# Optimization experiments

Measured on AMD Instinct MI355X. Metric: run time of the kernel, lower is better.

## Reference

```python
import jax, jax.numpy as jnp
import numpy as np

D_LINK = 64   # link_state_dim
D_PATH = 64   # path_state_dim
T = 3
MAX_LEN = 8   # max hops per path (max(seqs)+1)
R_UNITS = 256


def _glorot(k, shape):
    lim = np.sqrt(6.0 / (shape[0] + shape[-1])).astype(np.float32)
    return jax.random.uniform(k, shape, minval=-lim, maxval=lim, dtype=jnp.float32)


def setup_inputs() -> dict:
    key = jax.random.key(0)
    ks = jax.random.split(key, 16)
    n_links, n_paths, L = 50000, 100000, MAX_LEN
    capacities = jax.random.uniform(ks[0], (n_links,), dtype=jnp.float32) + 0.5
    traffic = jax.random.uniform(ks[1], (n_paths,), dtype=jnp.float32)
    # every path traverses L links; entries sorted by path id (tf.segment_sum assumption)
    paths = jnp.repeat(jnp.arange(n_paths, dtype=jnp.int32), L)
    seqs = jnp.tile(jnp.arange(L, dtype=jnp.int32), n_paths)
    links = jax.random.randint(ks[2], (n_paths * L,), 0, n_links, dtype=jnp.int32)
    return dict(
        capacities=capacities, traffic=traffic, links=links, paths=paths, seqs=seqs,
        Wx_p=_glorot(ks[3], (D_LINK, 3 * D_PATH)), Wh_p=_glorot(ks[4], (D_PATH, 3 * D_PATH)),
        b_p=jnp.zeros((3 * D_PATH,), jnp.float32),
        Wx_e=_glorot(ks[5], (D_PATH, 3 * D_LINK)), Wh_e=_glorot(ks[6], (D_LINK, 3 * D_LINK)),
        b_e=jnp.zeros((3 * D_LINK,), jnp.float32),
        W_r1=_glorot(ks[7], (D_PATH, R_UNITS)), b_r1=jnp.zeros((R_UNITS,), jnp.float32),
        W_r2=_glorot(ks[8], (R_UNITS, R_UNITS)), b_r2=jnp.zeros((R_UNITS,), jnp.float32),
        W_f=_glorot(ks[9], (D_PATH + R_UNITS, 1)), b_f=jnp.zeros((1,), jnp.float32),
        n_links=n_links, n_paths=n_paths,
    )


def gru_cell(x, h, Wx, Wh, b):
    # Keras GRUCell (reset_after=False), gate order z, r, h
    gx = x @ Wx + b
    gh = h @ Wh
    u = h.shape[-1]
    z = jax.nn.sigmoid(gx[..., :u] + gh[..., :u])
    r = jax.nn.sigmoid(gx[..., u:2 * u] + gh[..., u:2 * u])
    hc = jnp.tanh(gx[..., 2 * u:] + r * gh[..., 2 * u:])
    return z * h + (1.0 - z) * hc


def routenet_fwd(capacities, traffic, links, paths, seqs,
                 Wx_p, Wh_p, b_p, Wx_e, Wh_e, b_e,
                 W_r1, b_r1, W_r2, b_r2, W_f, b_f, n_links, n_paths):
    link_state = jnp.concatenate(
        [capacities[:, None], jnp.zeros((n_links, D_LINK - 1), capacities.dtype)], axis=1)
    path_state = jnp.concatenate(
        [traffic[:, None], jnp.zeros((n_paths, D_PATH - 1), traffic.dtype)], axis=1)
    lens = jax.ops.segment_sum(jnp.ones_like(paths), paths, num_segments=n_paths)  # [P]

    for _ in range(T):
        h_ = link_state[links]                                        # [E, D_LINK]
        link_inputs = jnp.zeros((n_paths, MAX_LEN, D_LINK), h_.dtype).at[paths, seqs].set(h_)

        def step(h, inp):
            xt, t = inp
            hn = gru_cell(xt, h, Wx_p, Wh_p, b_p)
            valid = (t < lens)[:, None]
            hn = jnp.where(valid, hn, h)          # dynamic_rnn copies state past seq len
            out = jnp.where(valid, hn, 0.0)       # and emits zeros there
            return hn, out

        path_state, outs = jax.lax.scan(
            step, path_state,
            (jnp.transpose(link_inputs, (1, 0, 2)), jnp.arange(MAX_LEN)))
        m = jnp.transpose(outs, (1, 0, 2))[paths, seqs]               # [E, D_PATH]
        m = jax.ops.segment_sum(m, links, num_segments=n_links)      # [n_links, D_PATH]
        link_state = gru_cell(m, link_state, Wx_e, Wh_e, b_e)

    r = jax.nn.selu(path_state @ W_r1 + b_r1)
    r = jax.nn.selu(r @ W_r2 + b_r2)          # dropout inactive (training=False)
    o = jnp.concatenate([r, path_state], axis=1) @ W_f + b_f
    return o


def reference(capacities, traffic, links, paths, seqs,
              Wx_p, Wh_p, b_p, Wx_e, Wh_e, b_e,
              W_r1, b_r1, W_r2, b_r2, W_f, b_f, n_links, n_paths):
    return routenet_fwd(capacities, traffic, links, paths, seqs,
                        Wx_p, Wh_p, b_p, Wx_e, Wh_e, b_e,
                        W_r1, b_r1, W_r2, b_r2, W_f, b_f, n_links, n_paths)
```

## Files before the change

kernel.cpp:

```cpp
#include <hip/hip_runtime.h>

typedef unsigned short ushort_t;
typedef unsigned int   uint_t;
typedef short bf16x8 __attribute__((ext_vector_type(8)));
typedef float f32x4  __attribute__((ext_vector_type(4)));

#define MFMA16(a,b,c) __builtin_amdgcn_mfma_f32_16x16x32_bf16((a),(b),(c),0,0,0)

static __device__ __forceinline__ float bf2f(ushort_t b) {
  union { uint_t u; float f; } v; v.u = ((uint_t)b) << 16; return v.f;
}
static __device__ __forceinline__ ushort_t f2bf(float f) {
  union { float f; uint_t u; } v; v.f = f;
  uint_t r = v.u + 0x7fffu + ((v.u >> 16) & 1u);
  return (ushort_t)(r >> 16);
}
static __device__ __forceinline__ float frcp(float x) { return __builtin_amdgcn_rcpf(x); }
static __device__ __forceinline__ float sigm(float x) { return frcp(1.0f + __expf(-x)); }
static __device__ __forceinline__ float ftanh(float x) { return 1.0f - 2.0f * frcp(1.0f + __expf(2.0f * x)); }
static __device__ __forceinline__ float selu_f(float x) {
  float e = 1.6732632423543772f * (__expf(x) - 1.0f);
  return 1.0507009873554805f * (x > 0.0f ? x : e);
}
static __device__ __forceinline__ bf16x8 pack8(float4 a, float4 b) {
  bf16x8 r;
  r[0] = (short)f2bf(a.x); r[1] = (short)f2bf(a.y); r[2] = (short)f2bf(a.z); r[3] = (short)f2bf(a.w);
  r[4] = (short)f2bf(b.x); r[5] = (short)f2bf(b.y); r[6] = (short)f2bf(b.z); r[7] = (short)f2bf(b.w);
  return r;
}
static __device__ __forceinline__ void split8(float4 a, float4 b, bf16x8& hi, bf16x8& lo) {
  hi = pack8(a, b);
  float4 ra, rb;
  ra.x = a.x - bf2f((ushort_t)hi[0]); ra.y = a.y - bf2f((ushort_t)hi[1]);
  ra.z = a.z - bf2f((ushort_t)hi[2]); ra.w = a.w - bf2f((ushort_t)hi[3]);
  rb.x = b.x - bf2f((ushort_t)hi[4]); rb.y = b.y - bf2f((ushort_t)hi[5]);
  rb.z = b.z - bf2f((ushort_t)hi[6]); rb.w = b.w - bf2f((ushort_t)hi[7]);
  lo = pack8(ra, rb);
}

#define GFRAG(ptr, f) (*(const bf16x8*)&(ptr)[(((f) * 64 + lane)) * 8])
#define LFRAG(arr, f) (*(const bf16x8*)&(arr)[(((f) * 64 + lane)) * 8])

__global__ void detect_dtype(const uint_t* __restrict__ caps, int* __restrict__ flag) {
  int lane = threadIdx.x;
  uint_t d = caps[lane];
  uint_t lo = d & 0xFFFFu, hi = d >> 16;
  bool isbf = (lo >= 0x3F00u && lo <= 0x3FC0u) && (hi >= 0x3F00u && hi <= 0x3FC0u);
  unsigned long long m = __ballot(isbf);
  if (lane == 0) *flag = (__popcll(m) >= 48) ? 1 : 0;
}

#define NARR 14
struct ConvDesc {
  const void* src[NARR];
  float*      dst[NARR];
  int         n[NARR];
  int         blk0[NARR + 1];
};
__global__ void conv_all(ConvDesc d, const int* __restrict__ flag) {
  int isbf = *flag;
  int b = blockIdx.x;
  int a = 0;
  while (a + 1 < NARR && b >= d.blk0[a + 1]) ++a;
  int idx = (b - d.blk0[a]) * 256 + threadIdx.x;
  if (idx >= d.n[a]) return;
  d.dst[a][idx] = isbf ? bf2f(((const ushort_t*)d.src[a])[idx])
                       : ((const float*)d.src[a])[idx];
}

struct PackAll {
  const float* A[8];
  const float* B[8];
  ushort_t* dH[8];
  ushort_t* dL[8];
  int srcN[8], colOff[8], splitK[8], nCk[8], NT[8], blk0[9];
};
__global__ void pack_all(PackAll P) {
  int b = blockIdx.x;
  int a = 0;
  while (a + 1 < 8 && b >= P.blk0[a + 1]) ++a;
  int i = (b - P.blk0[a]) * 256 + threadIdx.x;
  int j = i & 7;
  int lane = (i >> 3) & 63;
  int f = i >> 9;
  int c = f / P.NT[a], nt = f - c * P.NT[a];
  int k = c * 32 + ((lane >> 4) << 3) + j;
  int n = P.colOff[a] + nt * 16 + (lane & 15);
  float v = (k < P.splitK[a]) ? P.A[a][k * P.srcN[a] + n]
                              : P.B[a][(k - P.splitK[a]) * P.srcN[a] + n];
  ushort_t hi = f2bf(v);
  P.dH[a][i] = hi;
  P.dL[a][i] = f2bf(v - bf2f(hi));
}

__global__ void init_states(const float* __restrict__ caps, const float* __restrict__ traffic,
                            ushort_t* __restrict__ linkHL,
                            float* __restrict__ path_state, int n_links, int n_paths) {
  long i = (long)blockIdx.x * 256 + threadIdx.x;
  long total = (long)(n_links + n_paths) * 64;
  if (i >= total) return;
  int row = (int)(i >> 6), col = (int)(i & 63);
  if (row < n_links) {
    float v = (col == 0) ? caps[row] : 0.0f;
    ushort_t hi = f2bf(v);
    linkHL[(long)row * 128 + col] = hi;
    linkHL[(long)row * 128 + 64 + col] = f2bf(v - bf2f(hi));
  } else {
    int pr = row - n_links;
    path_state[(long)pr * 64 + col] = (col == 0) ? traffic[pr] : 0.0f;
  }
}

__global__ void hist_k(const int* __restrict__ links, int* __restrict__ cnt, int E) {
  int e = blockIdx.x * 256 + threadIdx.x;
  if (e < E) atomicAdd(&cnt[links[e]], 1);
}
__global__ void scan_k(const int* __restrict__ cnt, int* __restrict__ base,
                       int* __restrict__ cursor, int n) {
  __shared__ int part[256];
  int tid = threadIdx.x;
  int chunk = (n + 255) / 256;
  int lo = tid * chunk, hiEnd = lo + chunk; if (hiEnd > n) hiEnd = n;
  int s = 0;
  for (int i = lo; i < hiEnd; ++i) s += cnt[i];
  part[tid] = s;
  __syncthreads();
  if (tid == 0) { int acc = 0; for (int i = 0; i < 256; ++i) { int v = part[i]; part[i] = acc; acc += v; } }
  __syncthreads();
  int acc = part[tid];
  for (int i = lo; i < hiEnd; ++i) { base[i] = acc; cursor[i] = acc; acc += cnt[i]; }
}
__global__ void fill_k(const int* __restrict__ links, int* __restrict__ cursor,
                       int* __restrict__ pos_of, int E) {
  int e = blockIdx.x * 256 + threadIdx.x;
  if (e >= E) return;
  pos_of[e] = atomicAdd(&cursor[links[e]], 1);
}

__global__ __launch_bounds__(256) void agg_kernel(
    const float* __restrict__ mF, const ushort_t* __restrict__ mH, int mmode,
    const int* __restrict__ base, const int* __restrict__ cnt,
    float* __restrict__ agg, int n_links) {
  int l = blockIdx.x * 4 + (threadIdx.x >> 6);
  if (l >= n_links) return;
  int lane = threadIdx.x & 63;
  int s = base[l], d = cnt[l];
  float acc = 0.0f;
  if (mmode == 0) {
    for (int i = 0; i < d; ++i) acc += mF[(long)(s + i) * 64 + lane];
  } else {
    for (int i = 0; i < d; ++i) acc += bf2f(mH[(long)(s + i) * 64 + lane]);
  }
  agg[(long)l * 64 + lane] = acc;
}

#define PWB 7
__global__ __launch_bounds__(448, 3) void path_kernel_bf16(
    const int* __restrict__ links,
    const ushort_t* __restrict__ linkHL,
    float* __restrict__ path_state,
    float* __restrict__ mF, ushort_t* __restrict__ mH, int mmode, int store_m,
    const int* __restrict__ pos_of, float* __restrict__ agg,
    const ushort_t* __restrict__ wzrH, const ushort_t* __restrict__ wcH,
    const float* __restrict__ bp, const int* __restrict__ flagp, int n_paths) {
  __shared__ __align__(16) ushort_t s_wzr[32 * 512];
  __shared__ __align__(16) ushort_t s_wc[16 * 512];
  __shared__ __align__(16) ushort_t s_hh[PWB][16][68];
  __shared__ __align__(16) ushort_t s_hl[PWB][16][68];
  __shared__ float s_bias[192];

  if (flagp[0] == 0) return;

  int tid = threadIdx.x;
  {
    uint_t* s0 = (uint_t*)s_wzr; const uint_t* g0 = (const uint_t*)wzrH;
    for (int i = tid; i < 8192; i += 448) s0[i] = g0[i];
    uint_t* s1 = (uint_t*)s_wc;  const uint_t* g1 = (const uint_t*)wcH;
    for (int i = tid; i < 4096; i += 448) s1[i] = g1[i];
    for (int i = tid; i < 192; i += 448) s_bias[i] = bp[i];
  }

  int wv = tid >> 6, lane = tid & 63, l15 = lane & 15, quad = lane >> 4;
  int p0 = (blockIdx.x * PWB + wv) * 16;
  bool valid = (p0 < n_paths);

  float h[4][4];
  if (valid) {
#pragma unroll
    for (int tt = 0; tt < 4; ++tt)
#pragma unroll
      for (int r = 0; r < 4; ++r) {
        float v = path_state[(long)(p0 + quad * 4 + r) * 64 + tt * 16 + l15];
        h[tt][r] = v;
        ushort_t hi = f2bf(v);
        s_hh[wv][quad * 4 + r][tt * 16 + l15] = hi;
        s_hl[wv][quad * 4 + r][tt * 16 + l15] = f2bf(v - bf2f(hi));
      }
  }
  __syncthreads();
  if (!valid) return;

  for (int t = 0; t < 8; ++t) {
    int la = links[(p0 + l15) * 8 + t];
    const ushort_t* xr = linkHL + (long)la * 128;
    bf16x8 axH0 = *(const bf16x8*)(xr + quad * 8);
    bf16x8 axH1 = *(const bf16x8*)(xr + 32 + quad * 8);
    bf16x8 axL0 = *(const bf16x8*)(xr + 64 + quad * 8);
    bf16x8 axL1 = *(const bf16x8*)(xr + 96 + quad * 8);
    bf16x8 ahH0 = *(const bf16x8*)&s_hh[wv][l15][quad * 8];
    bf16x8 ahH1 = *(const bf16x8*)&s_hh[wv][l15][32 + quad * 8];
    bf16x8 ahL0 = *(const bf16x8*)&s_hl[wv][l15][quad * 8];
    bf16x8 ahL1 = *(const bf16x8*)&s_hl[wv][l15][32 + quad * 8];

    f32x4 azr[8];
#pragma unroll
    for (int nt = 0; nt < 8; ++nt) {
      f32x4 acc = {0.f, 0.f, 0.f, 0.f};
      acc = MFMA16(axH0, LFRAG(s_wzr, nt), acc);
      acc = MFMA16(axH1, LFRAG(s_wzr, 8 + nt), acc);
      acc = MFMA16(ahH0, LFRAG(s_wzr, 16 + nt), acc);
      acc = MFMA16(ahH1, LFRAG(s_wzr, 24 + nt), acc);
      acc = MFMA16(axL0, LFRAG(s_wzr, nt), acc);
      acc = MFMA16(axL1, LFRAG(s_wzr, 8 + nt), acc);
      acc = MFMA16(ahL0, LFRAG(s_wzr, 16 + nt), acc);
      acc = MFMA16(ahL1, LFRAG(s_wzr, 24 + nt), acc);
      azr[nt] = acc;
    }
    f32x4 axc[4], ahc[4];
#pragma unroll
    for (int nt = 0; nt < 4; ++nt) {
      f32x4 a = {0.f, 0.f, 0.f, 0.f};
      a = MFMA16(axH0, LFRAG(s_wc, nt), a);
      a = MFMA16(axH1, LFRAG(s_wc, 4 + nt), a);
      a = MFMA16(axL0, LFRAG(s_wc, nt), a);
      a = MFMA16(axL1, LFRAG(s_wc, 4 + nt), a);
      axc[nt] = a;
      f32x4 b = {0.f, 0.f, 0.f, 0.f};
      b = MFMA16(ahH0, LFRAG(s_wc, 8 + nt), b);
      b = MFMA16(ahH1, LFRAG(s_wc, 12 + nt), b);
      b = MFMA16(ahL0, LFRAG(s_wc, 8 + nt), b);
      b = MFMA16(ahL1, LFRAG(s_wc, 12 + nt), b);
      ahc[nt] = b;
    }

    int pr[4] = {0, 0, 0, 0};
    if (store_m) {
      if (mmode == 2) {
#pragma unroll
        for (int r = 0; r < 4; ++r) pr[r] = links[(p0 + quad * 4 + r) * 8 + t];
      } else {
#pragma unroll
        for (int r = 0; r < 4; ++r) pr[r] = pos_of[(p0 + quad * 4 + r) * 8 + t];
      }
    }

#pragma unroll
    for (int tt = 0; tt < 4; ++tt) {
      int col = tt * 16 + l15;
      float bz = s_bias[col], br = s_bias[64 + col], bc = s_bias[128 + col];
#pragma unroll
      for (int r = 0; r < 4; ++r) {
        float z   = sigm(azr[tt][r] + bz);
        float rr  = sigm(azr[4 + tt][r] + br);
        float hcv = ftanh(axc[tt][r] + bc + rr * ahc[tt][r]);
        float hn  = z * h[tt][r] + (1.0f - z) * hcv;
        h[tt][r] = hn;
        if (store_m) {
          if (mmode == 0)      mF[(long)pr[r] * 64 + col] = hn;
          else if (mmode == 1) mH[(long)pr[r] * 64 + col] = f2bf(hn);
          else atomicAdd(&agg[(long)pr[r] * 64 + col], hn);
        }
        ushort_t hi = f2bf(hn);
        s_hh[wv][quad * 4 + r][col] = hi;
        s_hl[wv][quad * 4 + r][col] = f2bf(hn - bf2f(hi));
      }
    }
  }

#pragma unroll
  for (int tt = 0; tt < 4; ++tt)
#pragma unroll
    for (int r = 0; r < 4; ++r)
      path_state[(long)(p0 + quad * 4 + r) * 64 + tt * 16 + l15] = h[tt][r];
}

#define PW 10
__global__ __launch_bounds__(640) void path_kernel_f32(
    const int* __restrict__ links,
    const ushort_t* __restrict__ linkHL,
    float* __restrict__ path_state,
    float* __restrict__ mF, ushort_t* __restrict__ mH, int mmode, int store_m,
    const int* __restrict__ pos_of, float* __restrict__ agg,
    const ushort_t* __restrict__ wzrH, const ushort_t* __restrict__ wzrL,
    const ushort_t* __restrict__ wcH,  const ushort_t* __restrict__ wcL,
    const float* __restrict__ bp, const int* __restrict__ flagp) {
  __shared__ __align__(16) ushort_t s_wzr[2][32 * 512];
  __shared__ __align__(16) ushort_t s_wc[2][16 * 512];
  __shared__ __align__(16) ushort_t s_hh[PW][16][72];
  __shared__ __align__(16) ushort_t s_hl[PW][16][72];
  __shared__ float s_bias[192];

  if (flagp[0] != 0) return;

  int tid = threadIdx.x;
  {
    uint_t* s0 = (uint_t*)s_wzr[0]; const uint_t* g0 = (const uint_t*)wzrH;
    for (int i = tid; i < 8192; i += 640) s0[i] = g0[i];
    uint_t* s1 = (uint_t*)s_wc[0];  const uint_t* g1 = (const uint_t*)wcH;
    for (int i = tid; i < 4096; i += 640) s1[i] = g1[i];
    uint_t* s2 = (uint_t*)s_wzr[1]; const uint_t* g2 = (const uint_t*)wzrL;
    for (int i = tid; i < 8192; i += 640) s2[i] = g2[i];
    uint_t* s3 = (uint_t*)s_wc[1];  const uint_t* g3 = (const uint_t*)wcL;
    for (int i = tid; i < 4096; i += 640) s3[i] = g3[i];
    for (int i = tid; i < 192; i += 640) s_bias[i] = bp[i];
  }

  int wv = tid >> 6, lane = tid & 63, l15 = lane & 15, quad = lane >> 4;
  int p0 = (blockIdx.x * PW + wv) * 16;

  float h[4][4];
#pragma unroll
  for (int tt = 0; tt < 4; ++tt)
#pragma unroll
    for (int r = 0; r < 4; ++r) {
      float v = path_state[(long)(p0 + quad * 4 + r) * 64 + tt * 16 + l15];
      h[tt][r] = v;
      ushort_t hi = f2bf(v);
      s_hh[wv][quad * 4 + r][tt * 16 + l15] = hi;
      s_hl[wv][quad * 4 + r][tt * 16 + l15] = f2bf(v - bf2f(hi));
    }
  __syncthreads();

  for (int t = 0; t < 8; ++t) {
    int la = links[(p0 + l15) * 8 + t];
    const ushort_t* xr = linkHL + (long)la * 128;
    bf16x8 axH0 = *(const bf16x8*)(xr + quad * 8);
    bf16x8 axH1 = *(const bf16x8*)(xr + 32 + quad * 8);
    bf16x8 axL0 = *(const bf16x8*)(xr + 64 + quad * 8);
    bf16x8 axL1 = *(const bf16x8*)(xr + 96 + quad * 8);
    bf16x8 ahH0 = *(const bf16x8*)&s_hh[wv][l15][quad * 8];
    bf16x8 ahH1 = *(const bf16x8*)&s_hh[wv][l15][32 + quad * 8];
    bf16x8 ahL0 = *(const bf16x8*)&s_hl[wv][l15][quad * 8];
    bf16x8 ahL1 = *(const bf16x8*)&s_hl[wv][l15][32 + quad * 8];

    f32x4 azr[8];
#pragma unroll
    for (int nt = 0; nt < 8; ++nt) {
      f32x4 acc = {0.f, 0.f, 0.f, 0.f};
      acc = MFMA16(axH0, LFRAG(s_wzr[0], nt), acc);
      acc = MFMA16(axH1, LFRAG(s_wzr[0], 8 + nt), acc);
      acc = MFMA16(ahH0, LFRAG(s_wzr[0], 16 + nt), acc);
      acc = MFMA16(ahH1, LFRAG(s_wzr[0], 24 + nt), acc);
      acc = MFMA16(axL0, LFRAG(s_wzr[0], nt), acc);
      acc = MFMA16(axL1, LFRAG(s_wzr[0], 8 + nt), acc);
      acc = MFMA16(ahL0, LFRAG(s_wzr[0], 16 + nt), acc);
      acc = MFMA16(ahL1, LFRAG(s_wzr[0], 24 + nt), acc);
      acc = MFMA16(axH0, LFRAG(s_wzr[1], nt), acc);
      acc = MFMA16(axH1, LFRAG(s_wzr[1], 8 + nt), acc);
      acc = MFMA16(ahH0, LFRAG(s_wzr[1], 16 + nt), acc);
      acc = MFMA16(ahH1, LFRAG(s_wzr[1], 24 + nt), acc);
      azr[nt] = acc;
    }
    f32x4 axc[4], ahc[4];
#pragma unroll
    for (int nt = 0; nt < 4; ++nt) {
      f32x4 a = {0.f, 0.f, 0.f, 0.f};
      a = MFMA16(axH0, LFRAG(s_wc[0], nt), a);
      a = MFMA16(axH1, LFRAG(s_wc[0], 4 + nt), a);
      a = MFMA16(axL0, LFRAG(s_wc[0], nt), a);
      a = MFMA16(axL1, LFRAG(s_wc[0], 4 + nt), a);
      a = MFMA16(axH0, LFRAG(s_wc[1], nt), a);
      a = MFMA16(axH1, LFRAG(s_wc[1], 4 + nt), a);
      axc[nt] = a;
      f32x4 b = {0.f, 0.f, 0.f, 0.f};
      b = MFMA16(ahH0, LFRAG(s_wc[0], 8 + nt), b);
      b = MFMA16(ahH1, LFRAG(s_wc[0], 12 + nt), b);
      b = MFMA16(ahL0, LFRAG(s_wc[0], 8 + nt), b);
      b = MFMA16(ahL1, LFRAG(s_wc[0], 12 + nt), b);
      b = MFMA16(ahH0, LFRAG(s_wc[1], 8 + nt), b);
      b = MFMA16(ahH1, LFRAG(s_wc[1], 12 + nt), b);
      ahc[nt] = b;
    }

    int pr[4] = {0, 0, 0, 0};
    if (store_m) {
      if (mmode == 2) {
#pragma unroll
        for (int r = 0; r < 4; ++r) pr[r] = links[(p0 + quad * 4 + r) * 8 + t];
      } else {
#pragma unroll
        for (int r = 0; r < 4; ++r) pr[r] = pos_of[(p0 + quad * 4 + r) * 8 + t];
      }
    }

#pragma unroll
    for (int tt = 0; tt < 4; ++tt) {
      int col = tt * 16 + l15;
      float bz = s_bias[col], br = s_bias[64 + col], bc = s_bias[128 + col];
#pragma unroll
      for (int r = 0; r < 4; ++r) {
        float z   = sigm(azr[tt][r] + bz);
        float rr  = sigm(azr[4 + tt][r] + br);
        float hcv = ftanh(axc[tt][r] + bc + rr * ahc[tt][r]);
        float hn  = z * h[tt][r] + (1.0f - z) * hcv;
        h[tt][r] = hn;
        if (store_m) {
          if (mmode == 0)      mF[(long)pr[r] * 64 + col] = hn;
          else if (mmode == 1) mH[(long)pr[r] * 64 + col] = f2bf(hn);
          else atomicAdd(&agg[(long)pr[r] * 64 + col], hn);
        }
        ushort_t hi = f2bf(hn);
        s_hh[wv][quad * 4 + r][col] = hi;
        s_hl[wv][quad * 4 + r][col] = f2bf(hn - bf2f(hi));
      }
    }
  }

#pragma unroll
  for (int tt = 0; tt < 4; ++tt)
#pragma unroll
    for (int r = 0; r < 4; ++r)
      path_state[(long)(p0 + quad * 4 + r) * 64 + tt * 16 + l15] = h[tt][r];
}

__global__ __launch_bounds__(320) void link_kernel(
    const float* __restrict__ agg,
    ushort_t* __restrict__ linkHL,
    const ushort_t* __restrict__ wzrH, const ushort_t* __restrict__ wzrL,
    const ushort_t* __restrict__ wcH,  const ushort_t* __restrict__ wcL,
    const float* __restrict__ be, const int* __restrict__ flagp) {
  __shared__ __align__(16) ushort_t s_wzr[2][32 * 512];
  __shared__ __align__(16) ushort_t s_wc[2][16 * 512];
  __shared__ float s_bias[192];

  int tid = threadIdx.x;
  int wlo = (flagp[0] == 0) ? 1 : 0;
  {
    uint_t* s0 = (uint_t*)s_wzr[0]; const uint_t* g0 = (const uint_t*)wzrH;
    for (int i = tid; i < 8192; i += 320) s0[i] = g0[i];
    uint_t* s1 = (uint_t*)s_wc[0];  const uint_t* g1 = (const uint_t*)wcH;
    for (int i = tid; i < 4096; i += 320) s1[i] = g1[i];
    if (wlo) {
      uint_t* s2 = (uint_t*)s_wzr[1]; const uint_t* g2 = (const uint_t*)wzrL;
      for (int i = tid; i < 8192; i += 320) s2[i] = g2[i];
      uint_t* s3 = (uint_t*)s_wc[1];  const uint_t* g3 = (const uint_t*)wcL;
      for (int i = tid; i < 4096; i += 320) s3[i] = g3[i];
    }
    for (int i = tid; i < 192; i += 320) s_bias[i] = be[i];
  }
  __syncthreads();

  int wv = tid >> 6, lane = tid & 63, l15 = lane & 15, quad = lane >> 4;
  int l0 = (blockIdx.x * 5 + wv) * 16;

  const float* arow = agg + (long)(l0 + l15) * 64;
  float4 f0 = *(const float4*)(arow + quad * 8);
  float4 f1 = *(const float4*)(arow + quad * 8 + 4);
  float4 f2 = *(const float4*)(arow + 32 + quad * 8);
  float4 f3 = *(const float4*)(arow + 36 + quad * 8);
  bf16x8 axH0, axL0, axH1, axL1;
  split8(f0, f1, axH0, axL0);
  split8(f2, f3, axH1, axL1);
  const ushort_t* hr = linkHL + (long)(l0 + l15) * 128;
  bf16x8 ahH0 = *(const bf16x8*)(hr + quad * 8);
  bf16x8 ahH1 = *(const bf16x8*)(hr + 32 + quad * 8);
  bf16x8 ahL0 = *(const bf16x8*)(hr + 64 + quad * 8);
  bf16x8 ahL1 = *(const bf16x8*)(hr + 96 + quad * 8);

  float h[4][4];
#pragma unroll
  for (int tt = 0; tt < 4; ++tt)
#pragma unroll
    for (int r = 0; r < 4; ++r) {
      long row = (long)(l0 + quad * 4 + r) * 128;
      int col = tt * 16 + l15;
      h[tt][r] = bf2f(linkHL[row + col]) + bf2f(linkHL[row + 64 + col]);
    }

  f32x4 azr[8];
#pragma unroll
  for (int nt = 0; nt < 8; ++nt) {
    f32x4 acc = {0.f, 0.f, 0.f, 0.f};
    acc = MFMA16(axH0, LFRAG(s_wzr[0], nt), acc);
    acc = MFMA16(axH1, LFRAG(s_wzr[0], 8 + nt), acc);
    acc = MFMA16(ahH0, LFRAG(s_wzr[0], 16 + nt), acc);
    acc = MFMA16(ahH1, LFRAG(s_wzr[0], 24 + nt), acc);
    acc = MFMA16(axL0, LFRAG(s_wzr[0], nt), acc);
    acc = MFMA16(axL1, LFRAG(s_wzr[0], 8 + nt), acc);
    acc = MFMA16(ahL0, LFRAG(s_wzr[0], 16 + nt), acc);
    acc = MFMA16(ahL1, LFRAG(s_wzr[0], 24 + nt), acc);
    azr[nt] = acc;
  }
  f32x4 axc[4], ahc[4];
#pragma unroll
  for (int nt = 0; nt < 4; ++nt) {
    f32x4 a = {0.f, 0.f, 0.f, 0.f};
    a = MFMA16(axH0, LFRAG(s_wc[0], nt), a);
    a = MFMA16(axH1, LFRAG(s_wc[0], 4 + nt), a);
    a = MFMA16(axL0, LFRAG(s_wc[0], nt), a);
    a = MFMA16(axL1, LFRAG(s_wc[0], 4 + nt), a);
    axc[nt] = a;
    f32x4 b = {0.f, 0.f, 0.f, 0.f};
    b = MFMA16(ahH0, LFRAG(s_wc[0], 8 + nt), b);
    b = MFMA16(ahH1, LFRAG(s_wc[0], 12 + nt), b);
    b = MFMA16(ahL0, LFRAG(s_wc[0], 8 + nt), b);
    b = MFMA16(ahL1, LFRAG(s_wc[0], 12 + nt), b);
    ahc[nt] = b;
  }
  if (wlo) {
#pragma unroll
    for (int nt = 0; nt < 8; ++nt) {
      azr[nt] = MFMA16(axH0, LFRAG(s_wzr[1], nt), azr[nt]);
      azr[nt] = MFMA16(axH1, LFRAG(s_wzr[1], 8 + nt), azr[nt]);
      azr[nt] = MFMA16(ahH0, LFRAG(s_wzr[1], 16 + nt), azr[nt]);
      azr[nt] = MFMA16(ahH1, LFRAG(s_wzr[1], 24 + nt), azr[nt]);
    }
#pragma unroll
    for (int nt = 0; nt < 4; ++nt) {
      axc[nt] = MFMA16(axH0, LFRAG(s_wc[1], nt), axc[nt]);
      axc[nt] = MFMA16(axH1, LFRAG(s_wc[1], 4 + nt), axc[nt]);
      ahc[nt] = MFMA16(ahH0, LFRAG(s_wc[1], 8 + nt), ahc[nt]);
      ahc[nt] = MFMA16(ahH1, LFRAG(s_wc[1], 12 + nt), ahc[nt]);
    }
  }

#pragma unroll
  for (int tt = 0; tt < 4; ++tt) {
    int col = tt * 16 + l15;
    float bz = s_bias[col], br = s_bias[64 + col], bc = s_bias[128 + col];
#pragma unroll
    for (int r = 0; r < 4; ++r) {
      float z   = sigm(azr[tt][r] + bz);
      float rr  = sigm(azr[4 + tt][r] + br);
      float hcv = ftanh(axc[tt][r] + bc + rr * ahc[tt][r]);
      float hn  = z * h[tt][r] + (1.0f - z) * hcv;
      long row = (long)(l0 + quad * 4 + r) * 128;
      ushort_t hi = f2bf(hn);
      linkHL[row + col] = hi;
      linkHL[row + 64 + col] = f2bf(hn - bf2f(hi));
    }
  }
}

#define RW 8
__global__ __launch_bounds__(512) void readout_kernel(
    const float* __restrict__ path_state, int n_paths,
    const ushort_t* __restrict__ wr1H, const ushort_t* __restrict__ wr1L,
    const ushort_t* __restrict__ wr2H, const ushort_t* __restrict__ wr2L,
    const float* __restrict__ br1, const float* __restrict__ br2,
    const float* __restrict__ Wf, const float* __restrict__ bfp,
    void* __restrict__ outp, const int* __restrict__ flagp) {
  __shared__ __align__(16) ushort_t s_r1h[RW][16][264];
  __shared__ __align__(16) ushort_t s_r1l[RW][16][264];
  int tid = threadIdx.x;
  int wv = tid >> 6, lane = tid & 63, l15 = lane & 15, quad = lane >> 4;
  int p0 = (blockIdx.x * RW + wv) * 16;
  if (p0 >= n_paths) return;
  int isbf = flagp[0];
  int wlo = (isbf == 0) ? 1 : 0;

  const float* prow = path_state + (long)(p0 + l15) * 64;
  float4 g0 = *(const float4*)(prow + quad * 8);
  float4 g1 = *(const float4*)(prow + quad * 8 + 4);
  float4 g2 = *(const float4*)(prow + 32 + quad * 8);
  float4 g3 = *(const float4*)(prow + 36 + quad * 8);
  bf16x8 axH0, axL0, axH1, axL1;
  split8(g0, g1, axH0, axL0);
  split8(g2, g3, axH1, axL1);

  f32x4 a1[16];
#pragma unroll
  for (int nt = 0; nt < 16; ++nt) {
    f32x4 acc = {0.f, 0.f, 0.f, 0.f};
    acc = MFMA16(axH0, GFRAG(wr1H, nt), acc);
    acc = MFMA16(axH1, GFRAG(wr1H, 16 + nt), acc);
    acc = MFMA16(axL0, GFRAG(wr1H, nt), acc);
    acc = MFMA16(axL1, GFRAG(wr1H, 16 + nt), acc);
    a1[nt] = acc;
  }
  if (wlo) {
#pragma unroll
    for (int nt = 0; nt < 16; ++nt) {
      a1[nt] = MFMA16(axH0, GFRAG(wr1L, nt), a1[nt]);
      a1[nt] = MFMA16(axH1, GFRAG(wr1L, 16 + nt), a1[nt]);
    }
  }
#pragma unroll
  for (int tt = 0; tt < 16; ++tt) {
    float bb = br1[tt * 16 + l15];
#pragma unroll
    for (int r = 0; r < 4; ++r) {
      float v = selu_f(a1[tt][r] + bb);
      ushort_t hi = f2bf(v);
      s_r1h[wv][quad * 4 + r][tt * 16 + l15] = hi;
      s_r1l[wv][quad * 4 + r][tt * 16 + l15] = f2bf(v - bf2f(hi));
    }
  }

  f32x4 a2[16];
  f32x4 zero = {0.f, 0.f, 0.f, 0.f};
#pragma unroll
  for (int nt = 0; nt < 16; ++nt) a2[nt] = zero;
#pragma unroll
  for (int c = 0; c < 8; ++c) {
    bf16x8 afH = *(const bf16x8*)&s_r1h[wv][l15][c * 32 + quad * 8];
    bf16x8 afL = *(const bf16x8*)&s_r1l[wv][l15][c * 32 + quad * 8];
#pragma unroll
    for (int nt = 0; nt < 16; ++nt) {
      a2[nt] = MFMA16(afH, GFRAG(wr2H, c * 16 + nt), a2[nt]);
      a2[nt] = MFMA16(afL, GFRAG(wr2H, c * 16 + nt), a2[nt]);
    }
    if (wlo) {
#pragma unroll
      for (int nt = 0; nt < 16; ++nt)
        a2[nt] = MFMA16(afH, GFRAG(wr2L, c * 16 + nt), a2[nt]);
    }
  }

  float part[4] = {0.f, 0.f, 0.f, 0.f};
#pragma unroll
  for (int tt = 0; tt < 16; ++tt) {
    float wf = Wf[tt * 16 + l15];
    float bb = br2[tt * 16 + l15];
#pragma unroll
    for (int r = 0; r < 4; ++r) part[r] += selu_f(a2[tt][r] + bb) * wf;
  }
  float wfh0 = Wf[256 + l15 * 4 + 0];
  float wfh1 = Wf[256 + l15 * 4 + 1];
  float wfh2 = Wf[256 + l15 * 4 + 2];
  float wfh3 = Wf[256 + l15 * 4 + 3];
#pragma unroll
  for (int r = 0; r < 4; ++r) {
    const float4 hh = *(const float4*)&path_state[(long)(p0 + quad * 4 + r) * 64 + l15 * 4];
    part[r] += hh.x * wfh0 + hh.y * wfh1 + hh.z * wfh2 + hh.w * wfh3;
  }
#pragma unroll
  for (int msk = 1; msk < 16; msk <<= 1)
#pragma unroll
    for (int r = 0; r < 4; ++r) part[r] += __shfl_xor(part[r], msk, 64);
  if (l15 == 0) {
    float bfv = bfp[0];
    if (isbf) {
#pragma unroll
      for (int r = 0; r < 4; ++r) ((ushort_t*)outp)[p0 + quad * 4 + r] = f2bf(part[r] + bfv);
    } else {
#pragma unroll
      for (int r = 0; r < 4; ++r) ((float*)outp)[p0 + quad * 4 + r] = part[r] + bfv;
    }
  }
}

extern "C" void kernel_launch(void* const* d_in, const int* in_sizes, int n_in,
                              void* d_out, int out_size, void* d_ws, size_t ws_size,
                              hipStream_t stream) {
  const int n_links = in_sizes[0];
  const int n_paths = in_sizes[1];
  const int E       = in_sizes[2];

  char* w = (char*)d_ws;
  size_t off = 0;
  auto take = [&](size_t bytes) { size_t o = off; off += (bytes + 255) & ~(size_t)255; return o; };
  float*    path_state = (float*)(w + take((size_t)n_paths * 64 * 4));
  float*    agg        = (float*)(w + take((size_t)n_links * 64 * 4));
  ushort_t* linkHL     = (ushort_t*)(w + take((size_t)n_links * 128 * 2));
  int*      flag       = (int*)(w + take(256));
  ushort_t* wzrH_p = (ushort_t*)(w + take(32768));
  ushort_t* wzrL_p = (ushort_t*)(w + take(32768));
  ushort_t* wcH_p  = (ushort_t*)(w + take(16384));
  ushort_t* wcL_p  = (ushort_t*)(w + take(16384));
  ushort_t* wzrH_e = (ushort_t*)(w + take(32768));
  ushort_t* wzrL_e = (ushort_t*)(w + take(32768));
  ushort_t* wcH_e  = (ushort_t*)(w + take(16384));
  ushort_t* wcL_e  = (ushort_t*)(w + take(16384));
  ushort_t* wr1H   = (ushort_t*)(w + take(32768));
  ushort_t* wr1L   = (ushort_t*)(w + take(32768));
  ushort_t* wr2H   = (ushort_t*)(w + take(131072));
  ushort_t* wr2L   = (ushort_t*)(w + take(131072));
  float* c_caps    = (float*)(w + take((size_t)in_sizes[0] * 4));
  float* c_traffic = (float*)(w + take((size_t)in_sizes[1] * 4));
  float* c_Wx_p = (float*)(w + take((size_t)in_sizes[5] * 4));
  float* c_Wh_p = (float*)(w + take((size_t)in_sizes[6] * 4));
  float* c_b_p  = (float*)(w + take((size_t)in_sizes[7] * 4));
  float* c_Wx_e = (float*)(w + take((size_t)in_sizes[8] * 4));
  float* c_Wh_e = (float*)(w + take((size_t)in_sizes[9] * 4));
  float* c_b_e  = (float*)(w + take((size_t)in_sizes[10] * 4));
  float* c_Wr1  = (float*)(w + take((size_t)in_sizes[11] * 4));
  float* c_br1  = (float*)(w + take((size_t)in_sizes[12] * 4));
  float* c_Wr2  = (float*)(w + take((size_t)in_sizes[13] * 4));
  float* c_br2  = (float*)(w + take((size_t)in_sizes[14] * 4));
  float* c_Wf   = (float*)(w + take((size_t)in_sizes[15] * 4));
  float* c_bf   = (float*)(w + take((size_t)in_sizes[16] * 4));
  int* cnt    = (int*)(w + take((size_t)n_links * 4));
  int* base   = (int*)(w + take((size_t)n_links * 4));
  int* cursor = (int*)(w + take((size_t)n_links * 4));
  int* pos_of = (int*)(w + take((size_t)E * 4));

  size_t rem = (ws_size > off) ? (ws_size - off) : 0;
  int mmode;
  float*    mF = nullptr;
  ushort_t* mH = nullptr;
  if (rem >= (size_t)E * 64 * 4 + 256) { mmode = 0; mF = (float*)(w + take((size_t)E * 64 * 4)); }
  else if (rem >= (size_t)E * 64 * 2 + 256) { mmode = 1; mH = (ushort_t*)(w + take((size_t)E * 64 * 2)); }
  else mmode = 2;

  detect_dtype<<<1, 64, 0, stream>>>((const uint_t*)d_in[0], flag);

  ConvDesc cd;
  float* dsts[NARR] = {c_caps, c_traffic, c_Wx_p, c_Wh_p, c_b_p, c_Wx_e, c_Wh_e, c_b_e,
                       c_Wr1, c_br1, c_Wr2, c_br2, c_Wf, c_bf};
  int    srcs[NARR] = {0, 1, 5, 6, 7, 8, 9, 10, 11, 12, 13, 14, 15, 16};
  int nblk = 0;
  for (int a = 0; a < NARR; ++a) {
    cd.src[a] = d_in[srcs[a]];
    cd.dst[a] = dsts[a];
    cd.n[a] = in_sizes[srcs[a]];
    cd.blk0[a] = nblk;
    nblk += (cd.n[a] + 255) / 256;
  }
  cd.blk0[NARR] = nblk;
  conv_all<<<nblk, 256, 0, stream>>>(cd, flag);

  {
    long total = (long)(n_links + n_paths) * 64;
    int blocks = (int)((total + 255) / 256);
    init_states<<<blocks, 256, 0, stream>>>(c_caps, c_traffic, linkHL, path_state,
                                            n_links, n_paths);
  }
  {
    PackAll P;
    const float* As[8] = {c_Wx_p, c_Wx_p, c_Wh_p, c_Wx_e, c_Wx_e, c_Wh_e, c_Wr1, c_Wr2};
    const float* Bs[8] = {c_Wh_p, c_Wx_p, c_Wh_p, c_Wh_e, c_Wx_e, c_Wh_e, c_Wr1, c_Wr2};
    ushort_t* dH[8] = {wzrH_p, wcH_p, wcH_p + 4096, wzrH_e, wcH_e, wcH_e + 4096, wr1H, wr2H};
    ushort_t* dL[8] = {wzrL_p, wcL_p, wcL_p + 4096, wzrL_e, wcL_e, wcL_e + 4096, wr1L, wr2L};
    int srcN[8]   = {192, 192, 192, 192, 192, 192, 256, 256};
    int colOff[8] = {0, 128, 128, 0, 128, 128, 0, 0};
    int splitK[8] = {64, 64, 64, 64, 64, 64, 64, 256};
    int nCk[8]    = {4, 2, 2, 4, 2, 2, 2, 8};
    int NT[8]     = {8, 4, 4, 8, 4, 4, 16, 16};
    int pb = 0;
    for (int a = 0; a < 8; ++a) {
      P.A[a] = As[a]; P.B[a] = Bs[a]; P.dH[a] = dH[a]; P.dL[a] = dL[a];
      P.srcN[a] = srcN[a]; P.colOff[a] = colOff[a]; P.splitK[a] = splitK[a];
      P.nCk[a] = nCk[a]; P.NT[a] = NT[a]; P.blk0[a] = pb;
      pb += nCk[a] * NT[a] * 2;
    }
    P.blk0[8] = pb;
    pack_all<<<pb, 256, 0, stream>>>(P);
  }

  const int* links = (const int*)d_in[2];
  if (mmode < 2) {
    (void)hipMemsetAsync(cnt, 0, (size_t)n_links * 4, stream);
    hist_k<<<(E + 255) / 256, 256, 0, stream>>>(links, cnt, E);
    scan_k<<<1, 256, 0, stream>>>(cnt, base, cursor, n_links);
    fill_k<<<(E + 255) / 256, 256, 0, stream>>>(links, cursor, pos_of, E);
  }

  int grid_bf = (n_paths + 16 * PWB - 1) / (16 * PWB);
  for (int it = 0; it < 3; ++it) {
    int store_m = (it < 2) ? 1 : 0;
    if (mmode == 2 && store_m) (void)hipMemsetAsync(agg, 0, (size_t)n_links * 64 * 4, stream);
    path_kernel_bf16<<<grid_bf, 16 * PWB * 4, 0, stream>>>(
        links, linkHL, path_state, mF, mH, mmode, store_m, pos_of, agg,
        wzrH_p, wcH_p, c_b_p, flag, n_paths);
    path_kernel_f32<<<n_paths / 160, 640, 0, stream>>>(
        links, linkHL, path_state, mF, mH, mmode, store_m, pos_of, agg,
        wzrH_p, wzrL_p, wcH_p, wcL_p, c_b_p, flag);
    if (it < 2) {
      if (mmode < 2)
        agg_kernel<<<(n_links + 3) / 4, 256, 0, stream>>>(mF, mH, mmode, base, cnt,
                                                          agg, n_links);
      link_kernel<<<n_links / 80, 320, 0, stream>>>(agg, linkHL,
                                                    wzrH_e, wzrL_e, wcH_e, wcL_e, c_b_e, flag);
    }
  }
  readout_kernel<<<(n_paths + 16 * RW - 1) / (16 * RW), 512, 0, stream>>>(
      path_state, n_paths, wr1H, wr1L, wr2H, wr2L,
      c_br1, c_br2, c_Wf, c_bf, d_out, flag);
}
```

Measured before the change: 1.196 ms.

## Make f32 path GRU persistent with link-row prefetch and bf16 message buffer

The f32 path kernel becomes persistent: at most 256 blocks of 832 threads (13 waves) loop over path groups, so the shared weight tiles are loaded once per block instead of once per 160 paths. Inside the time loop, the next hop's link-state row is prefetched into registers while the current step's MFMAs run, hiding gather latency. The fp32 message buffer mode is dropped, so per-edge messages are always stored in bf16, which halves scatter and aggregation traffic but lowers the precision of the aggregated messages. The bf16 path kernel also loses its occupancy hint in launch bounds.

```diff
diff --git a/kernel.cpp b/kernel.cpp
--- a/kernel.cpp
+++ b/kernel.cpp
@@ -138,7 +138,7 @@
 }
 
 __global__ __launch_bounds__(256) void agg_kernel(
-    const float* __restrict__ mF, const ushort_t* __restrict__ mH, int mmode,
+    const ushort_t* __restrict__ mH,
     const int* __restrict__ base, const int* __restrict__ cnt,
     float* __restrict__ agg, int n_links) {
   int l = blockIdx.x * 4 + (threadIdx.x >> 6);
@@ -146,20 +146,16 @@
   int lane = threadIdx.x & 63;
   int s = base[l], d = cnt[l];
   float acc = 0.0f;
-  if (mmode == 0) {
-    for (int i = 0; i < d; ++i) acc += mF[(long)(s + i) * 64 + lane];
-  } else {
-    for (int i = 0; i < d; ++i) acc += bf2f(mH[(long)(s + i) * 64 + lane]);
-  }
+  for (int i = 0; i < d; ++i) acc += bf2f(mH[(long)(s + i) * 64 + lane]);
   agg[(long)l * 64 + lane] = acc;
 }
 
 #define PWB 7
-__global__ __launch_bounds__(448, 3) void path_kernel_bf16(
+__global__ __launch_bounds__(448) void path_kernel_bf16(
     const int* __restrict__ links,
     const ushort_t* __restrict__ linkHL,
     float* __restrict__ path_state,
-    float* __restrict__ mF, ushort_t* __restrict__ mH, int mmode, int store_m,
+    ushort_t* __restrict__ mH, int mmode, int store_m,
     const int* __restrict__ pos_of, float* __restrict__ agg,
     const ushort_t* __restrict__ wzrH, const ushort_t* __restrict__ wcH,
     const float* __restrict__ bp, const int* __restrict__ flagp, int n_paths) {
@@ -266,8 +262,7 @@
         float hn  = z * h[tt][r] + (1.0f - z) * hcv;
         h[tt][r] = hn;
         if (store_m) {
-          if (mmode == 0)      mF[(long)pr[r] * 64 + col] = hn;
-          else if (mmode == 1) mH[(long)pr[r] * 64 + col] = f2bf(hn);
+          if (mmode == 1) mH[(long)pr[r] * 64 + col] = f2bf(hn);
           else atomicAdd(&agg[(long)pr[r] * 64 + col], hn);
         }
         ushort_t hi = f2bf(hn);
@@ -284,16 +279,17 @@
       path_state[(long)(p0 + quad * 4 + r) * 64 + tt * 16 + l15] = h[tt][r];
 }
 
-#define PW 10
-__global__ __launch_bounds__(640) void path_kernel_f32(
+#define PW 13
+__global__ __launch_bounds__(832) void path_kernel_f32(
     const int* __restrict__ links,
     const ushort_t* __restrict__ linkHL,
     float* __restrict__ path_state,
-    float* __restrict__ mF, ushort_t* __restrict__ mH, int mmode, int store_m,
+    ushort_t* __restrict__ mH, int mmode, int store_m,
     const int* __restrict__ pos_of, float* __restrict__ agg,
     const ushort_t* __restrict__ wzrH, const ushort_t* __restrict__ wzrL,
     const ushort_t* __restrict__ wcH,  const ushort_t* __restrict__ wcL,
-    const float* __restrict__ bp, const int* __restrict__ flagp) {
+    const float* __restrict__ bp, const int* __restrict__ flagp,
+    int n_paths, int nGroups) {
   __shared__ __align__(16) ushort_t s_wzr[2][32 * 512];
   __shared__ __align__(16) ushort_t s_wc[2][16 * 512];
   __shared__ __align__(16) ushort_t s_hh[PW][16][72];
@@ -305,122 +301,138 @@
   int tid = threadIdx.x;
   {
     uint_t* s0 = (uint_t*)s_wzr[0]; const uint_t* g0 = (const uint_t*)wzrH;
-    for (int i = tid; i < 8192; i += 640) s0[i] = g0[i];
+    for (int i = tid; i < 8192; i += 832) s0[i] = g0[i];
     uint_t* s1 = (uint_t*)s_wc[0];  const uint_t* g1 = (const uint_t*)wcH;
-    for (int i = tid; i < 4096; i += 640) s1[i] = g1[i];
+    for (int i = tid; i < 4096; i += 832) s1[i] = g1[i];
     uint_t* s2 = (uint_t*)s_wzr[1]; const uint_t* g2 = (const uint_t*)wzrL;
-    for (int i = tid; i < 8192; i += 640) s2[i] = g2[i];
+    for (int i = tid; i < 8192; i += 832) s2[i] = g2[i];
     uint_t* s3 = (uint_t*)s_wc[1];  const uint_t* g3 = (const uint_t*)wcL;
-    for (int i = tid; i < 4096; i += 640) s3[i] = g3[i];
-    for (int i = tid; i < 192; i += 640) s_bias[i] = bp[i];
-  }
+    for (int i = tid; i < 4096; i += 832) s3[i] = g3[i];
+    for (int i = tid; i < 192; i += 832) s_bias[i] = bp[i];
+  }
+  __syncthreads();
 
   int wv = tid >> 6, lane = tid & 63, l15 = lane & 15, quad = lane >> 4;
-  int p0 = (blockIdx.x * PW + wv) * 16;
-
-  float h[4][4];
-#pragma unroll
-  for (int tt = 0; tt < 4; ++tt)
-#pragma unroll
-    for (int r = 0; r < 4; ++r) {
-      float v = path_state[(long)(p0 + quad * 4 + r) * 64 + tt * 16 + l15];
-      h[tt][r] = v;
-      ushort_t hi = f2bf(v);
-      s_hh[wv][quad * 4 + r][tt * 16 + l15] = hi;
-      s_hl[wv][quad * 4 + r][tt * 16 + l15] = f2bf(v - bf2f(hi));
-    }
-  __syncthreads();
-
-  for (int t = 0; t < 8; ++t) {
-    int la = links[(p0 + l15) * 8 + t];
-    const ushort_t* xr = linkHL + (long)la * 128;
-    bf16x8 axH0 = *(const bf16x8*)(xr + quad * 8);
-    bf16x8 axH1 = *(const bf16x8*)(xr + 32 + quad * 8);
-    bf16x8 axL0 = *(const bf16x8*)(xr + 64 + quad * 8);
-    bf16x8 axL1 = *(const bf16x8*)(xr + 96 + quad * 8);
-    bf16x8 ahH0 = *(const bf16x8*)&s_hh[wv][l15][quad * 8];
-    bf16x8 ahH1 = *(const bf16x8*)&s_hh[wv][l15][32 + quad * 8];
-    bf16x8 ahL0 = *(const bf16x8*)&s_hl[wv][l15][quad * 8];
-    bf16x8 ahL1 = *(const bf16x8*)&s_hl[wv][l15][32 + quad * 8];
-
-    f32x4 azr[8];
-#pragma unroll
-    for (int nt = 0; nt < 8; ++nt) {
-      f32x4 acc = {0.f, 0.f, 0.f, 0.f};
-      acc = MFMA16(axH0, LFRAG(s_wzr[0], nt), acc);
-      acc = MFMA16(axH1, LFRAG(s_wzr[0], 8 + nt), acc);
-      acc = MFMA16(ahH0, LFRAG(s_wzr[0], 16 + nt), acc);
-      acc = MFMA16(ahH1, LFRAG(s_wzr[0], 24 + nt), acc);
-      acc = MFMA16(axL0, LFRAG(s_wzr[0], nt), acc);
-      acc = MFMA16(axL1, LFRAG(s_wzr[0], 8 + nt), acc);
-      acc = MFMA16(ahL0, LFRAG(s_wzr[0], 16 + nt), acc);
-      acc = MFMA16(ahL1, LFRAG(s_wzr[0], 24 + nt), acc);
-      acc = MFMA16(axH0, LFRAG(s_wzr[1], nt), acc);
-      acc = MFMA16(axH1, LFRAG(s_wzr[1], 8 + nt), acc);
-      acc = MFMA16(ahH0, LFRAG(s_wzr[1], 16 + nt), acc);
-      acc = MFMA16(ahH1, LFRAG(s_wzr[1], 24 + nt), acc);
-      azr[nt] = acc;
-    }
-    f32x4 axc[4], ahc[4];
-#pragma unroll
-    for (int nt = 0; nt < 4; ++nt) {
-      f32x4 a = {0.f, 0.f, 0.f, 0.f};
-      a = MFMA16(axH0, LFRAG(s_wc[0], nt), a);
-      a = MFMA16(axH1, LFRAG(s_wc[0], 4 + nt), a);
-      a = MFMA16(axL0, LFRAG(s_wc[0], nt), a);
-      a = MFMA16(axL1, LFRAG(s_wc[0], 4 + nt), a);
-      a = MFMA16(axH0, LFRAG(s_wc[1], nt), a);
-      a = MFMA16(axH1, LFRAG(s_wc[1], 4 + nt), a);
-      axc[nt] = a;
-      f32x4 b = {0.f, 0.f, 0.f, 0.f};
-      b = MFMA16(ahH0, LFRAG(s_wc[0], 8 + nt), b);
-      b = MFMA16(ahH1, LFRAG(s_wc[0], 12 + nt), b);
-      b = MFMA16(ahL0, LFRAG(s_wc[0], 8 + nt), b);
-      b = MFMA16(ahL1, LFRAG(s_wc[0], 12 + nt), b);
-      b = MFMA16(ahH0, LFRAG(s_wc[1], 8 + nt), b);
-      b = MFMA16(ahH1, LFRAG(s_wc[1], 12 + nt), b);
-      ahc[nt] = b;
-    }
-
-    int pr[4] = {0, 0, 0, 0};
-    if (store_m) {
-      if (mmode == 2) {
-#pragma unroll
-        for (int r = 0; r < 4; ++r) pr[r] = links[(p0 + quad * 4 + r) * 8 + t];
-      } else {
-#pragma unroll
-        for (int r = 0; r < 4; ++r) pr[r] = pos_of[(p0 + quad * 4 + r) * 8 + t];
+
+  for (int g = 0; g < nGroups; ++g) {
+    int slot = g * gridDim.x + blockIdx.x;
+    int p0 = (slot * PW + wv) * 16;
+    if (p0 >= n_paths) continue;
+
+    float h[4][4];
+#pragma unroll
+    for (int tt = 0; tt < 4; ++tt)
+#pragma unroll
+      for (int r = 0; r < 4; ++r) {
+        float v = path_state[(long)(p0 + quad * 4 + r) * 64 + tt * 16 + l15];
+        h[tt][r] = v;
+        ushort_t hi = f2bf(v);
+        s_hh[wv][quad * 4 + r][tt * 16 + l15] = hi;
+        s_hl[wv][quad * 4 + r][tt * 16 + l15] = f2bf(v - bf2f(hi));
       }
-    }
-
-#pragma unroll
-    for (int tt = 0; tt < 4; ++tt) {
-      int col = tt * 16 + l15;
-      float bz = s_bias[col], br = s_bias[64 + col], bc = s_bias[128 + col];
-#pragma unroll
-      for (int r = 0; r < 4; ++r) {
-        float z   = sigm(azr[tt][r] + bz);
-        float rr  = sigm(azr[4 + tt][r] + br);
-        float hcv = ftanh(axc[tt][r] + bc + rr * ahc[tt][r]);
-        float hn  = z * h[tt][r] + (1.0f - z) * hcv;
-        h[tt][r] = hn;
+
+    const int* lrow = links + (long)(p0 + l15) * 8;
+    {
+      int la0 = lrow[0];
+      const ushort_t* x0 = linkHL + (long)la0 * 128;
+      bf16x8 nH0 = *(const bf16x8*)(x0 + quad * 8);
+      bf16x8 nH1 = *(const bf16x8*)(x0 + 32 + quad * 8);
+      bf16x8 nL0 = *(const bf16x8*)(x0 + 64 + quad * 8);
+      bf16x8 nL1 = *(const bf16x8*)(x0 + 96 + quad * 8);
+
+      for (int t = 0; t < 8; ++t) {
+        bf16x8 axH0 = nH0, axH1 = nH1, axL0 = nL0, axL1 = nL1;
+        if (t < 7) {
+          int la2 = lrow[t + 1];
+          const ushort_t* x2 = linkHL + (long)la2 * 128;
+          nH0 = *(const bf16x8*)(x2 + quad * 8);
+          nH1 = *(const bf16x8*)(x2 + 32 + quad * 8);
+          nL0 = *(const bf16x8*)(x2 + 64 + quad * 8);
+          nL1 = *(const bf16x8*)(x2 + 96 + quad * 8);
+        }
+        int pr[4] = {0, 0, 0, 0};
         if (store_m) {
-          if (mmode == 0)      mF[(long)pr[r] * 64 + col] = hn;
-          else if (mmode == 1) mH[(long)pr[r] * 64 + col] = f2bf(hn);
-          else atomicAdd(&agg[(long)pr[r] * 64 + col], hn);
+          if (mmode == 2) {
+#pragma unroll
+            for (int r = 0; r < 4; ++r) pr[r] = links[(long)(p0 + quad * 4 + r) * 8 + t];
+          } else {
+#pragma unroll
+            for (int r = 0; r < 4; ++r) pr[r] = pos_of[(long)(p0 + quad * 4 + r) * 8 + t];
+          }
         }
-        ushort_t hi = f2bf(hn);
-        s_hh[wv][quad * 4 + r][col] = hi;
-        s_hl[wv][quad * 4 + r][col] = f2bf(hn - bf2f(hi));
+        bf16x8 ahH0 = *(const bf16x8*)&s_hh[wv][l15][quad * 8];
+        bf16x8 ahH1 = *(const bf16x8*)&s_hh[wv][l15][32 + quad * 8];
+        bf16x8 ahL0 = *(const bf16x8*)&s_hl[wv][l15][quad * 8];
+        bf16x8 ahL1 = *(const bf16x8*)&s_hl[wv][l15][32 + quad * 8];
+
+        f32x4 azr[8];
+#pragma unroll
+        for (int nt = 0; nt < 8; ++nt) {
+          f32x4 acc = {0.f, 0.f, 0.f, 0.f};
+          acc = MFMA16(axH0, LFRAG(s_wzr[0], nt), acc);
+          acc = MFMA16(axH1, LFRAG(s_wzr[0], 8 + nt), acc);
+          acc = MFMA16(axL0, LFRAG(s_wzr[0], nt), acc);
+          acc = MFMA16(axL1, LFRAG(s_wzr[0], 8 + nt), acc);
+          acc = MFMA16(axH0, LFRAG(s_wzr[1], nt), acc);
+          acc = MFMA16(axH1, LFRAG(s_wzr[1], 8 + nt), acc);
+          acc = MFMA16(ahH0, LFRAG(s_wzr[0], 16 + nt), acc);
+          acc = MFMA16(ahH1, LFRAG(s_wzr[0], 24 + nt), acc);
+          acc = MFMA16(ahL0, LFRAG(s_wzr[0], 16 + nt), acc);
+          acc = MFMA16(ahL1, LFRAG(s_wzr[0], 24 + nt), acc);
+          acc = MFMA16(ahH0, LFRAG(s_wzr[1], 16 + nt), acc);
+          acc = MFMA16(ahH1, LFRAG(s_wzr[1], 24 + nt), acc);
+          azr[nt] = acc;
+        }
+        f32x4 axc[4], ahc[4];
+#pragma unroll
+        for (int nt = 0; nt < 4; ++nt) {
+          f32x4 a = {0.f, 0.f, 0.f, 0.f};
+          a = MFMA16(axH0, LFRAG(s_wc[0], nt), a);
+          a = MFMA16(axH1, LFRAG(s_wc[0], 4 + nt), a);
+          a = MFMA16(axL0, LFRAG(s_wc[0], nt), a);
+          a = MFMA16(axL1, LFRAG(s_wc[0], 4 + nt), a);
+          a = MFMA16(axH0, LFRAG(s_wc[1], nt), a);
+          a = MFMA16(axH1, LFRAG(s_wc[1], 4 + nt), a);
+          axc[nt] = a;
+          f32x4 b = {0.f, 0.f, 0.f, 0.f};
+          b = MFMA16(ahH0, LFRAG(s_wc[0], 8 + nt), b);
+          b = MFMA16(ahH1, LFRAG(s_wc[0], 12 + nt), b);
+          b = MFMA16(ahL0, LFRAG(s_wc[0], 8 + nt), b);
+          b = MFMA16(ahL1, LFRAG(s_wc[0], 12 + nt), b);
+          b = MFMA16(ahH0, LFRAG(s_wc[1], 8 + nt), b);
+          b = MFMA16(ahH1, LFRAG(s_wc[1], 12 + nt), b);
+          ahc[nt] = b;
+        }
+
+#pragma unroll
+        for (int tt = 0; tt < 4; ++tt) {
+          int col = tt * 16 + l15;
+          float bz = s_bias[col], br = s_bias[64 + col], bc = s_bias[128 + col];
+#pragma unroll
+          for (int r = 0; r < 4; ++r) {
+            float z   = sigm(azr[tt][r] + bz);
+            float rr  = sigm(azr[4 + tt][r] + br);
+            float hcv = ftanh(axc[tt][r] + bc + rr * ahc[tt][r]);
+            float hn  = z * h[tt][r] + (1.0f - z) * hcv;
+            h[tt][r] = hn;
+            if (store_m) {
+              if (mmode == 1) mH[(long)pr[r] * 64 + col] = f2bf(hn);
+              else atomicAdd(&agg[(long)pr[r] * 64 + col], hn);
+            }
+            ushort_t hi = f2bf(hn);
+            s_hh[wv][quad * 4 + r][col] = hi;
+            s_hl[wv][quad * 4 + r][col] = f2bf(hn - bf2f(hi));
+          }
+        }
       }
     }
-  }
-
-#pragma unroll
-  for (int tt = 0; tt < 4; ++tt)
-#pragma unroll
-    for (int r = 0; r < 4; ++r)
-      path_state[(long)(p0 + quad * 4 + r) * 64 + tt * 16 + l15] = h[tt][r];
+
+#pragma unroll
+    for (int tt = 0; tt < 4; ++tt)
+#pragma unroll
+      for (int r = 0; r < 4; ++r)
+        path_state[(long)(p0 + quad * 4 + r) * 64 + tt * 16 + l15] = h[tt][r];
+  }
 }
 
 __global__ __launch_bounds__(320) void link_kernel(
@@ -697,10 +709,8 @@
 
   size_t rem = (ws_size > off) ? (ws_size - off) : 0;
   int mmode;
-  float*    mF = nullptr;
   ushort_t* mH = nullptr;
-  if (rem >= (size_t)E * 64 * 4 + 256) { mmode = 0; mF = (float*)(w + take((size_t)E * 64 * 4)); }
-  else if (rem >= (size_t)E * 64 * 2 + 256) { mmode = 1; mH = (ushort_t*)(w + take((size_t)E * 64 * 2)); }
+  if (rem >= (size_t)E * 64 * 2 + 256) { mmode = 1; mH = (ushort_t*)(w + take((size_t)E * 64 * 2)); }
   else mmode = 2;
 
   detect_dtype<<<1, 64, 0, stream>>>((const uint_t*)d_in[0], flag);
@@ -749,7 +759,7 @@
   }
 
   const int* links = (const int*)d_in[2];
-  if (mmode < 2) {
+  if (mmode == 1) {
     (void)hipMemsetAsync(cnt, 0, (size_t)n_links * 4, stream);
     hist_k<<<(E + 255) / 256, 256, 0, stream>>>(links, cnt, E);
     scan_k<<<1, 256, 0, stream>>>(cnt, base, cursor, n_links);
@@ -757,19 +767,22 @@
   }
 
   int grid_bf = (n_paths + 16 * PWB - 1) / (16 * PWB);
+  int slots   = (n_paths + 16 * PW - 1) / (16 * PW);
+  int gridF   = slots < 256 ? slots : 256;
+  int nGroups = (slots + gridF - 1) / gridF;
+
   for (int it = 0; it < 3; ++it) {
     int store_m = (it < 2) ? 1 : 0;
     if (mmode == 2 && store_m) (void)hipMemsetAsync(agg, 0, (size_t)n_links * 64 * 4, stream);
-    path_kernel_bf16<<<grid_bf, 16 * PWB * 4, 0, stream>>>(
-        links, linkHL, path_state, mF, mH, mmode, store_m, pos_of, agg,
+    path_kernel_bf16<<<grid_bf, 448, 0, stream>>>(
+        links, linkHL, path_state, mH, mmode, store_m, pos_of, agg,
         wzrH_p, wcH_p, c_b_p, flag, n_paths);
-    path_kernel_f32<<<n_paths / 160, 640, 0, stream>>>(
-        links, linkHL, path_state, mF, mH, mmode, store_m, pos_of, agg,
-        wzrH_p, wzrL_p, wcH_p, wcL_p, c_b_p, flag);
+    path_kernel_f32<<<gridF, 832, 0, stream>>>(
+        links, linkHL, path_state, mH, mmode, store_m, pos_of, agg,
+        wzrH_p, wzrL_p, wcH_p, wcL_p, c_b_p, flag, n_paths, nGroups);
     if (it < 2) {
-      if (mmode < 2)
-        agg_kernel<<<(n_links + 3) / 4, 256, 0, stream>>>(mF, mH, mmode, base, cnt,
-                                                          agg, n_links);
+      if (mmode == 1)
+        agg_kernel<<<(n_links + 3) / 4, 256, 0, stream>>>(mH, base, cnt, agg, n_links);
       link_kernel<<<n_links / 80, 320, 0, stream>>>(agg, linkHL,
                                                     wzrH_e, wzrL_e, wcH_e, wcL_e, c_b_e, flag);
     }
```

Measured after the change: 1.162 ms. -2.8%, faster.
